# Performance work log

Measured on AMD Instinct MI355X. Metric: run time of the kernel, lower is better.

## Reference

```python
import jax, jax.numpy as jnp
import numpy as np

DIM = 4096
N_HEADS = 32
N_KV_HEADS = 8
HEAD_DIM = 128
ROPE_BASE = 10000.0
B, L = 4, 1024
NEG_INF = -1e9


def rope_traditional(x, base=ROPE_BASE, offset=0):
    # x: [B, H, L, Dh]; rotates interleaved pairs (x[...,2i], x[...,2i+1])
    Dh = x.shape[-1]
    Lx = x.shape[2]
    inv_freq = base ** (-jnp.arange(0, Dh, 2, dtype=jnp.float32) / Dh)  # [Dh/2]
    pos = jnp.arange(offset, offset + Lx, dtype=jnp.float32)
    ang = pos[:, None] * inv_freq  # [L, Dh/2]
    cos, sin = jnp.cos(ang), jnp.sin(ang)
    x1, x2 = x[..., ::2], x[..., 1::2]
    r1 = x1 * cos - x2 * sin
    r2 = x1 * sin + x2 * cos
    return jnp.stack([r1, r2], axis=-1).reshape(x.shape).astype(x.dtype)


def setup_inputs() -> dict:
    key = jax.random.key(0)
    ks = jax.random.split(key, 5)
    x = jax.random.normal(ks[0], (B, L, DIM), dtype=jnp.float32)
    # additive causal mask: 0 on/below diag, -inf-like above
    mask = jnp.where(jnp.tril(jnp.ones((L, L), dtype=bool)), 0.0, NEG_INF).astype(jnp.float32)
    wq = jax.random.normal(ks[1], (DIM, N_HEADS * HEAD_DIM), dtype=jnp.float32) * 0.02
    wk = jax.random.normal(ks[2], (DIM, N_KV_HEADS * HEAD_DIM), dtype=jnp.float32) * 0.02
    wv = jax.random.normal(ks[3], (DIM, N_KV_HEADS * HEAD_DIM), dtype=jnp.float32) * 0.02
    wo = jax.random.normal(ks[4], (N_HEADS * HEAD_DIM, DIM), dtype=jnp.float32) * 0.02
    return {"x": x, "mask": mask, "wq": wq, "wk": wk, "wv": wv, "wo": wo}


def reference(x, mask, wq, wk, wv, wo):
    Bx, Lx, D = x.shape
    scale = HEAD_DIM ** -0.5
    repeats = N_HEADS // N_KV_HEADS
    q = (x @ wq).reshape(Bx, Lx, N_HEADS, HEAD_DIM).transpose(0, 2, 1, 3)      # [B,H,L,Dh]
    k = (x @ wk).reshape(Bx, Lx, N_KV_HEADS, HEAD_DIM).transpose(0, 2, 1, 3)   # [B,Hkv,L,Dh]
    v = (x @ wv).reshape(Bx, Lx, N_KV_HEADS, HEAD_DIM).transpose(0, 2, 1, 3)
    # GQA expansion: head h attends to kv head h % n_kv_heads (matches
    # expand_dims+repeat(axis=1)+reshape in the original)
    k = jnp.tile(k, (1, repeats, 1, 1))  # [B,H,L,Dh]
    v = jnp.tile(v, (1, repeats, 1, 1))
    # cache=None path: rope with offset 0
    q = rope_traditional(q)
    k = rope_traditional(k)
    scores = jnp.einsum("bhqd,bhkd->bhqk", q * scale, k) + mask
    probs = jax.nn.softmax(scores.astype(jnp.float32), axis=-1).astype(scores.dtype)
    out = jnp.einsum("bhqk,bhkd->bhqd", probs, v)
    out = out.transpose(0, 2, 1, 3).reshape(Bx, Lx, D)
    return out @ wo
```

## Files before the change

### kernel.cpp

```cpp
#include <hip/hip_runtime.h>
#include <stdint.h>

typedef unsigned short u16;
typedef __bf16 bf16x8 __attribute__((ext_vector_type(8)));
typedef float f32x4 __attribute__((ext_vector_type(4)));

__device__ __forceinline__ u16 f2b(float x) {
  uint32_t b = __float_as_uint(x);
  b += 0x7fff + ((b >> 16) & 1);
  return (u16)(b >> 16);
}
__device__ __forceinline__ float b2f(u16 u) {
  return __uint_as_float(((uint32_t)u) << 16);
}

#define GLD16(src, dst)                                                                  \
  __builtin_amdgcn_global_load_lds((const __attribute__((address_space(1))) void*)(src),\
                                   (__attribute__((address_space(3))) void*)(dst), 16, 0, 0)

__device__ __forceinline__ f32x4 mfma16(bf16x8 a, bf16x8 b, f32x4 c) {
  return __builtin_amdgcn_mfma_f32_16x16x32_bf16(a, b, c, 0, 0, 0);
}

__global__ void k_rope_table(float2* __restrict__ tab) {
  int i = blockIdx.x * 256 + threadIdx.x;
  int l = i >> 6, d = i & 63;
  float inv = powf(10000.0f, -(float)(2 * d) / 128.0f);
  float ang = (float)l * inv;
  float s, c;
  sincosf(ang, &s, &c);
  tab[i] = make_float2(c, s);
}

__global__ void k_cast8(const float* __restrict__ src, u16* __restrict__ dst) {
  size_t i = (size_t)blockIdx.x * 256 + threadIdx.x;
  const float4* s4 = (const float4*)src;
  float4 a = s4[2 * i], b = s4[2 * i + 1];
  union { u16 u[8]; uint4 v; } o;
  o.u[0] = f2b(a.x); o.u[1] = f2b(a.y); o.u[2] = f2b(a.z); o.u[3] = f2b(a.w);
  o.u[4] = f2b(b.x); o.u[5] = f2b(b.y); o.u[6] = f2b(b.z); o.u[7] = f2b(b.w);
  ((uint4*)dst)[i] = o.v;
}

__global__ __launch_bounds__(256) void k_tcast(const float* __restrict__ src,
                                               u16* __restrict__ dst, int R, int C) {
  __shared__ u16 t[64][72];
  int tiles_c = C >> 6;
  int tr = blockIdx.x / tiles_c, tc = blockIdx.x % tiles_c;
  int tid = threadIdx.x;
  {
    int rr = tid >> 4, cv = tid & 15;
#pragma unroll
    for (int it = 0; it < 4; ++it) {
      int row = rr + it * 16;
      float4 v = *(const float4*)(src + (size_t)(tr * 64 + row) * C + tc * 64 + cv * 4);
      t[row][cv * 4 + 0] = f2b(v.x);
      t[row][cv * 4 + 1] = f2b(v.y);
      t[row][cv * 4 + 2] = f2b(v.z);
      t[row][cv * 4 + 3] = f2b(v.w);
    }
  }
  __syncthreads();
  {
    int cc = tid >> 3, g = tid & 7;
#pragma unroll
    for (int it = 0; it < 2; ++it) {
      int c = cc + it * 32;
      union { u16 u[8]; uint4 v; } o;
#pragma unroll
      for (int j = 0; j < 8; ++j) o.u[j] = t[g * 8 + j][c];
      *(uint4*)(dst + (size_t)(tc * 64 + c) * R + tr * 64 + g * 8) = o.v;
    }
  }
}

__global__ __launch_bounds__(256) void k_vtrans(const u16* __restrict__ qkv,
                                                u16* __restrict__ vrt) {
  __shared__ u16 t[64][72];
  int b = blockIdx.x >> 8;
  int tt = blockIdx.x & 255;
  int tr = tt >> 4, tc = tt & 15;
  int tid = threadIdx.x;
  {
    int rr = tid >> 3, g = tid & 7;
#pragma unroll
    for (int it = 0; it < 2; ++it) {
      int row = rr + it * 32;
      union { u16 u[8]; uint4 v; } o;
      o.v = *(const uint4*)(qkv + (size_t)(b * 1024 + tr * 64 + row) * 6144 + 5120 + tc * 64 + g * 8);
#pragma unroll
      for (int j = 0; j < 8; ++j) t[row][g * 8 + j] = o.u[j];
    }
  }
  __syncthreads();
  {
    int cc = tid >> 3, g = tid & 7;
#pragma unroll
    for (int it = 0; it < 2; ++it) {
      int c = cc + it * 32;
      union { u16 u[8]; uint4 v; } o;
#pragma unroll
      for (int j = 0; j < 8; ++j) o.u[j] = t[g * 8 + j][c];
      *(uint4*)(vrt + (size_t)(b * 1024 + tc * 64 + c) * 1024 + tr * 64 + g * 8) = o.v;
    }
  }
}

__global__ __launch_bounds__(320) void k_rope8(const u16* __restrict__ qkv,
                                               const float2* __restrict__ tab,
                                               u16* __restrict__ qr, u16* __restrict__ kr) {
  int row = blockIdx.x;
  int j = threadIdx.x * 8;
  int b = row >> 10, l = row & 1023;
  const float qs = 0.12751586584003446f;
  bool isq = (j < 2048);
  int jj = isq ? j : (j - 2048);
  int h = jj >> 6, dp = jj & 63;
  const u16* src = qkv + (size_t)row * 6144 + (isq ? 0 : 4096) + h * 128 + 2 * dp;
  uint4 v0 = *(const uint4*)(src);
  uint4 v1 = *(const uint4*)(src + 8);
  const float2* tb = tab + l * 64 + dp;
  float sc = isq ? qs : 1.0f;
  union { u16 u[16]; uint4 v[2]; } o;
  const uint32_t* w = (const uint32_t*)&v0;
#pragma unroll
  for (int i = 0; i < 8; ++i) {
    uint32_t pair = (i < 4) ? w[i] : ((const uint32_t*)&v1)[i - 4];
    float2 cs = tb[i];
    float x1 = b2f((u16)pair), x2 = b2f((u16)(pair >> 16));
    float r1 = (x1 * cs.x - x2 * cs.y) * sc;
    float r2 = (x1 * cs.y + x2 * cs.x) * sc;
    o.u[2 * i] = f2b(r1);
    o.u[2 * i + 1] = f2b(r2);
  }
  u16* dst = isq ? (qr + ((size_t)((b * 32 + h) * 1024 + l)) * 128 + 2 * dp)
                 : (kr + ((size_t)((b * 8 + h) * 1024 + l)) * 128 + 2 * dp);
  *(uint4*)(dst) = o.v[0];
  *(uint4*)(dst + 8) = o.v[1];
}

#define STAGE2(s0, s1, koff, ldsoff)          \
  GLD16((s0) + (koff), dst0 + (ldsoff));      \
  GLD16((s1) + (koff), dst1 + (ldsoff));

#define LOADB(base, kh)                                                   \
  bfr[0] = *(const bf16x8*)((base) + (kh) * 8192 + 0 * 512);              \
  bfr[1] = *(const bf16x8*)((base) + (kh) * 8192 + 1 * 512);              \
  bfr[2] = *(const bf16x8*)((base) + (kh) * 8192 + 2 * 512);              \
  bfr[3] = *(const bf16x8*)((base) + (kh) * 8192 + 3 * 512);

#define LOADA(base, kh, mh)                                               \
  afr[0] = *(const bf16x8*)((base) + (kh) * 8192 + (mh) * 2048 + 0 * 512);\
  afr[1] = *(const bf16x8*)((base) + (kh) * 8192 + (mh) * 2048 + 1 * 512);\
  afr[2] = *(const bf16x8*)((base) + (kh) * 8192 + (mh) * 2048 + 2 * 512);\
  afr[3] = *(const bf16x8*)((base) + (kh) * 8192 + (mh) * 2048 + 3 * 512);

#define PH(mh)                                                            \
  __builtin_amdgcn_s_barrier();                                           \
  asm volatile("s_waitcnt lgkmcnt(0)" ::: "memory");                      \
  __builtin_amdgcn_s_setprio(1);                                          \
  _Pragma("unroll") for (int mm = 0; mm < 4; ++mm)                        \
    _Pragma("unroll") for (int n_ = 0; n_ < 4; ++n_)                      \
      acc[(mh) * 4 + mm][n_] = mfma16(afr[mm], bfr[n_], acc[(mh) * 4 + mm][n_]); \
  __builtin_amdgcn_s_setprio(0);                                          \
  __builtin_amdgcn_s_barrier();

#define VMC(n) asm volatile("s_waitcnt vmcnt(" #n ")" ::: "memory");

template <typename OutT>
__global__ __launch_bounds__(512, 2) void k_gemm8(const u16* __restrict__ A,
                                                  const u16* __restrict__ Bt,
                                                  OutT* __restrict__ C,
                                                  int M, int N, int K) {
  extern __shared__ u16 lds[];
  const int tid = threadIdx.x;
  const int lane = tid & 63, wid = tid >> 6;
  const int l16 = lane & 15, lhi = lane >> 4;
  const int wm = wid >> 2, wn = wid & 3;

  const int nbn = N >> 8;
  int bid = blockIdx.x;
  const int cpx = gridDim.x >> 3;
  bid = (bid & 7) * cpx + (bid >> 3);
  const int bm = (bid / nbn) << 8;
  const int bn = (bid % nbn) << 8;

  const u16* Ag = A + (size_t)bm * K;
  const u16* Bg = Bt + (size_t)bn * K;

  const int swz = (lhi ^ ((l16 >> 1) & 3)) << 3;
  const u16* pA0 = lds + wm * 4096 + l16 * 32 + swz;
  const u16* pA1 = pA0 + 32768;
  const u16* pB0 = lds + 16384 + wn * 2048 + l16 * 32 + swz;
  const u16* pB1 = pB0 + 32768;

  const int r0 = tid >> 2, g0 = tid & 3;
  const int r1 = r0 + 128;
  const size_t so0 = (size_t)r0 * K + ((g0 ^ ((r0 >> 1) & 3)) << 3);
  const size_t so1 = (size_t)r1 * K + ((g0 ^ ((r1 >> 1) & 3)) << 3);
  const u16* sA0 = Ag + so0;
  const u16* sA1 = Ag + so1;
  const u16* sB0 = Bg + so0;
  const u16* sB1 = Bg + so1;
  u16* dst0 = lds + wid * 512;
  u16* dst1 = lds + 4096 + wid * 512;

  f32x4 acc[8][4] = {};
  bf16x8 bfr[4], afr[4];

  STAGE2(sA0, sA1, 0, 0);
  STAGE2(sA0, sA1, 32, 8192);
  STAGE2(sB0, sB1, 0, 16384);
  STAGE2(sB0, sB1, 32, 24576);
  STAGE2(sB0, sB1, 64, 49152);
  STAGE2(sA0, sA1, 64, 32768);
  STAGE2(sB0, sB1, 96, 57344);
  VMC(6)
  __builtin_amdgcn_s_barrier();

  const int nt = K >> 6;
  for (int t = 0; t < nt - 2; t += 2) {
    const int kA1 = (t + 1) * 64 + 32;
    const int k2 = (t + 2) * 64;
    const int k3 = (t + 3) * 64;
    LOADB(pB0, 0)
    LOADA(pA0, 0, 0)
    STAGE2(sA0, sA1, kA1, 40960);
    PH(0)
    LOADA(pA0, 0, 1)
    STAGE2(sB0, sB1, k2, 16384);
    PH(1)
    LOADB(pB0, 1)
    LOADA(pA0, 1, 0)
    STAGE2(sA0, sA1, k2, 0);
    PH(0)
    LOADA(pA0, 1, 1)
    STAGE2(sB0, sB1, k2 + 32, 24576);
    VMC(6)
    PH(1)
    LOADB(pB1, 0)
    LOADA(pA1, 0, 0)
    STAGE2(sA0, sA1, k2 + 32, 8192);
    PH(0)
    LOADA(pA1, 0, 1)
    STAGE2(sB0, sB1, k3, 49152);
    PH(1)
    LOADB(pB1, 1)
    LOADA(pA1, 1, 0)
    STAGE2(sA0, sA1, k3, 32768);
    PH(0)
    LOADA(pA1, 1, 1)
    STAGE2(sB0, sB1, k3 + 32, 57344);
    VMC(6)
    PH(1)
  }
  {
    const int kA1 = (nt - 1) * 64 + 32;
    LOADB(pB0, 0)
    LOADA(pA0, 0, 0)
    STAGE2(sA0, sA1, kA1, 40960);
    PH(0)
    LOADA(pA0, 0, 1)
    PH(1)
    LOADB(pB0, 1)
    LOADA(pA0, 1, 0)
    PH(0)
    LOADA(pA0, 1, 1)
    VMC(0)
    PH(1)
    LOADB(pB1, 0)
    LOADA(pA1, 0, 0)
    PH(0)
    LOADA(pA1, 0, 1)
    PH(1)
    LOADB(pB1, 1)
    LOADA(pA1, 1, 0)
    PH(0)
    LOADA(pA1, 1, 1)
    PH(1)
  }

#pragma unroll
  for (int m = 0; m < 8; ++m) {
    int row = bm + wm * 128 + m * 16 + lhi * 4;
#pragma unroll
    for (int n = 0; n < 4; ++n) {
      int col = bn + wn * 64 + n * 16 + l16;
#pragma unroll
      for (int r = 0; r < 4; ++r) {
        float v = acc[m][n][r];
        size_t idx = (size_t)(row + r) * N + col;
        if constexpr (sizeof(OutT) == 2) C[idx] = f2b(v);
        else C[idx] = v;
      }
    }
  }
}

__global__ __launch_bounds__(512) void k_attn(const u16* __restrict__ qr,
                                              const u16* __restrict__ kr,
                                              const u16* __restrict__ vrt,
                                              u16* __restrict__ ao) {
  __shared__ u16 Klds[8192];
  __shared__ u16 Vlds[8192];
  __shared__ u16 Plds[9216];
  int bid = blockIdx.x;
  int qb = bid & 7, h = (bid >> 3) & 31, b = bid >> 8;
  int kvh = h & 7;
  int lane = threadIdx.x & 63, w = threadIdx.x >> 6;
  int l16 = lane & 15, lhi = lane >> 4;
  int qmin = qb * 128 + w * 16;

  const u16* qbase = qr + ((size_t)((b * 32 + h) * 1024) + qmin + l16) * 128;
  bf16x8 aq[4];
#pragma unroll
  for (int kc = 0; kc < 4; ++kc) aq[kc] = *(const bf16x8*)(qbase + kc * 32 + lhi * 8);

  const u16* Kg = kr + (size_t)(b * 8 + kvh) * (1024 * 128);
  const u16* Vg = vrt + (size_t)(b * 8 + kvh) * (128 * 1024);

  float m_run[4] = {-1e30f, -1e30f, -1e30f, -1e30f};
  float l_part[4] = {0.f, 0.f, 0.f, 0.f};
  f32x4 o[8] = {};

  int nkb = 2 * qb + 2;
  for (int kb = 0; kb < nkb; ++kb) {
    int kv0 = kb * 64;
#pragma unroll
    for (int i = 0; i < 2; ++i) {
      int c = w * 128 + i * 64 + lane;
      int krow = c >> 4, g = c & 15;
      GLD16(Kg + (size_t)(kv0 + krow) * 128 + ((g ^ (krow & 7)) * 8),
            Klds + (w * 128 + i * 64) * 8);
    }
#pragma unroll
    for (int i = 0; i < 2; ++i) {
      int c = w * 128 + i * 64 + lane;
      int d = c >> 3, g = c & 7;
      GLD16(Vg + (size_t)d * 1024 + kv0 + ((g ^ (d & 7)) * 8),
            Vlds + (w * 128 + i * 64) * 8);
    }
    __syncthreads();

    f32x4 s[4] = {};
#pragma unroll
    for (int kc = 0; kc < 4; ++kc) {
#pragma unroll
      for (int n = 0; n < 4; ++n) {
        int kv = n * 16 + l16;
        int g = kc * 4 + lhi;
        bf16x8 bk = *(const bf16x8*)(Klds + kv * 128 + ((g ^ (kv & 7)) * 8));
        s[n] = mfma16(aq[kc], bk, s[n]);
      }
    }
    if (kv0 + 63 > qmin) {
#pragma unroll
      for (int n = 0; n < 4; ++n)
#pragma unroll
        for (int r = 0; r < 4; ++r) {
          int q = qmin + lhi * 4 + r;
          int kv = kv0 + n * 16 + l16;
          if (kv > q) s[n][r] = -1e30f;
        }
    }
    float mx[4];
    bool need = false;
#pragma unroll
    for (int r = 0; r < 4; ++r) {
      float m0 = fmaxf(fmaxf(s[0][r], s[1][r]), fmaxf(s[2][r], s[3][r]));
      m0 = fmaxf(m0, __shfl_xor(m0, 1));
      m0 = fmaxf(m0, __shfl_xor(m0, 2));
      m0 = fmaxf(m0, __shfl_xor(m0, 4));
      m0 = fmaxf(m0, __shfl_xor(m0, 8));
      mx[r] = m0;
      need = need || (m0 > m_run[r] + 11.0f);
    }
    if (__any(need)) {
#pragma unroll
      for (int r = 0; r < 4; ++r) {
        float mn = fmaxf(m_run[r], mx[r]);
        float sf = exp2f(m_run[r] - mn);
        m_run[r] = mn;
        l_part[r] *= sf;
#pragma unroll
        for (int nd = 0; nd < 8; ++nd) o[nd][r] *= sf;
      }
    }
    u16* pw = Plds + w * 1152;
#pragma unroll
    for (int r = 0; r < 4; ++r) {
      float lsum = 0.f;
#pragma unroll
      for (int n = 0; n < 4; ++n) {
        float p = exp2f(s[n][r] - m_run[r]);
        lsum += p;
        pw[(lhi * 4 + r) * 72 + n * 16 + l16] = f2b(p);
      }
      l_part[r] += lsum;
    }
#pragma unroll
    for (int kc = 0; kc < 2; ++kc) {
      bf16x8 ap = *(const bf16x8*)(pw + l16 * 72 + kc * 32 + lhi * 8);
#pragma unroll
      for (int nd = 0; nd < 8; ++nd) {
        int d = nd * 16 + l16;
        int g = kc * 4 + lhi;
        bf16x8 bv = *(const bf16x8*)(Vlds + d * 64 + ((g ^ (d & 7)) * 8));
        o[nd] = mfma16(ap, bv, o[nd]);
      }
    }
    __syncthreads();
  }
#pragma unroll
  for (int r = 0; r < 4; ++r) {
    float l = l_part[r];
    l += __shfl_xor(l, 1);
    l += __shfl_xor(l, 2);
    l += __shfl_xor(l, 4);
    l += __shfl_xor(l, 8);
    float inv = 1.0f / l;
    int q = qmin + lhi * 4 + r;
    u16* orow = ao + ((size_t)(b * 1024 + q)) * 4096 + h * 128;
#pragma unroll
    for (int nd = 0; nd < 8; ++nd) orow[nd * 16 + l16] = f2b(o[nd][r] * inv);
  }
}

extern "C" void kernel_launch(void* const* d_in, const int* in_sizes, int n_in,
                              void* d_out, int out_size, void* d_ws, size_t ws_size,
                              hipStream_t stream) {
  const float* x = (const float*)d_in[0];
  const float* wq = (const float*)d_in[2];
  const float* wk = (const float*)d_in[3];
  const float* wv = (const float*)d_in[4];
  const float* wo = (const float*)d_in[5];

  char* ws = (char*)d_ws;
  u16* xb = (u16*)(ws + 0);
  u16* wcat = (u16*)(ws + 33554432);
  u16* qr = (u16*)(ws + 0);
  u16* kr = (u16*)(ws + 33554432);
  u16* vrt = (u16*)(ws + 41943040);
  u16* ao = (u16*)(ws + 50331648);
  u16* wob = (u16*)(ws + 83886080);
  float2* tab = (float2*)(ws + 117440512);
  u16* qkv = (u16*)d_out;

  hipFuncSetAttribute((const void*)k_gemm8<u16>,
                      hipFuncAttributeMaxDynamicSharedMemorySize, 131072);
  hipFuncSetAttribute((const void*)k_gemm8<float>,
                      hipFuncAttributeMaxDynamicSharedMemorySize, 131072);

  k_rope_table<<<256, 256, 0, stream>>>(tab);
  k_cast8<<<8192, 256, 0, stream>>>(x, xb);
  k_tcast<<<4096, 256, 0, stream>>>(wq, wcat, 4096, 4096);
  k_tcast<<<1024, 256, 0, stream>>>(wk, wcat + (size_t)4096 * 4096, 4096, 1024);
  k_tcast<<<1024, 256, 0, stream>>>(wv, wcat + (size_t)5120 * 4096, 4096, 1024);
  k_tcast<<<4096, 256, 0, stream>>>(wo, wob, 4096, 4096);
  k_gemm8<u16><<<384, 512, 131072, stream>>>(xb, wcat, qkv, 4096, 6144, 4096);
  k_rope8<<<4096, 320, 0, stream>>>(qkv, tab, qr, kr);
  k_vtrans<<<1024, 256, 0, stream>>>(qkv, vrt);
  k_attn<<<1024, 512, 0, stream>>>(qr, kr, vrt, ao);
  k_gemm8<float><<<256, 512, 131072, stream>>>(ao, wob, (float*)d_out, 4096, 4096, 4096);
}
```

Before: 541.2 us.

## Double-buffer K tiles in LDS and read V directly from global memory

Loads of K tiles into LDS are now double-buffered: the next tile is prefetched while the current one is used, with a waitcnt and barrier at the end of each iteration. V is no longer staged in LDS and is read straight from global memory inside the PV MFMA loop, which frees the V buffer's LDS space. This hides K load latency and removes one barrier per iteration. In exchange, V reads become uncached-in-LDS global loads sitting on the MFMA critical path, repeated by every wave.

```diff
diff --git a/kernel.cpp b/kernel.cpp
--- a/kernel.cpp
+++ b/kernel.cpp
@@ -301,8 +301,7 @@
                                               const u16* __restrict__ kr,
                                               const u16* __restrict__ vrt,
                                               u16* __restrict__ ao) {
-  __shared__ u16 Klds[8192];
-  __shared__ u16 Vlds[8192];
+  __shared__ u16 Klds[16384];
   __shared__ u16 Plds[9216];
   int bid = blockIdx.x;
   int qb = bid & 7, h = (bid >> 3) & 31, b = bid >> 8;
@@ -319,28 +318,33 @@
   const u16* Kg = kr + (size_t)(b * 8 + kvh) * (1024 * 128);
   const u16* Vg = vrt + (size_t)(b * 8 + kvh) * (128 * 1024);
 
+  const int c0 = w * 128 + lane;
+  const int kr0 = c0 >> 4, g0s = c0 & 15;
+  const int c1 = c0 + 64;
+  const int kr1 = c1 >> 4, g1s = c1 & 15;
+  const size_t ko0 = (size_t)kr0 * 128 + ((g0s ^ (kr0 & 7)) * 8);
+  const size_t ko1 = (size_t)kr1 * 128 + ((g1s ^ (kr1 & 7)) * 8);
+  u16* kd0 = Klds + c0 * 8;
+  u16* kd1 = Klds + c1 * 8;
+
   float m_run[4] = {-1e30f, -1e30f, -1e30f, -1e30f};
   float l_part[4] = {0.f, 0.f, 0.f, 0.f};
   f32x4 o[8] = {};
 
   int nkb = 2 * qb + 2;
+  GLD16(Kg + ko0, kd0);
+  GLD16(Kg + ko1, kd1);
+  asm volatile("s_waitcnt vmcnt(0)" ::: "memory");
+  __builtin_amdgcn_s_barrier();
+
   for (int kb = 0; kb < nkb; ++kb) {
     int kv0 = kb * 64;
-#pragma unroll
-    for (int i = 0; i < 2; ++i) {
-      int c = w * 128 + i * 64 + lane;
-      int krow = c >> 4, g = c & 15;
-      GLD16(Kg + (size_t)(kv0 + krow) * 128 + ((g ^ (krow & 7)) * 8),
-            Klds + (w * 128 + i * 64) * 8);
-    }
-#pragma unroll
-    for (int i = 0; i < 2; ++i) {
-      int c = w * 128 + i * 64 + lane;
-      int d = c >> 3, g = c & 7;
-      GLD16(Vg + (size_t)d * 1024 + kv0 + ((g ^ (d & 7)) * 8),
-            Vlds + (w * 128 + i * 64) * 8);
-    }
-    __syncthreads();
+    const u16* Kb = Klds + (kb & 1) * 8192;
+    int nb = ((kb & 1) ^ 1) * 8192;
+    if (kb + 1 < nkb) {
+      GLD16(Kg + (size_t)(kv0 + 64) * 128 + ko0, kd0 + nb);
+      GLD16(Kg + (size_t)(kv0 + 64) * 128 + ko1, kd1 + nb);
+    }
 
     f32x4 s[4] = {};
 #pragma unroll
@@ -349,7 +353,7 @@
       for (int n = 0; n < 4; ++n) {
         int kv = n * 16 + l16;
         int g = kc * 4 + lhi;
-        bf16x8 bk = *(const bf16x8*)(Klds + kv * 128 + ((g ^ (kv & 7)) * 8));
+        bf16x8 bk = *(const bf16x8*)(Kb + kv * 128 + ((g ^ (kv & 7)) * 8));
         s[n] = mfma16(aq[kc], bk, s[n]);
       }
     }
@@ -404,12 +408,12 @@
 #pragma unroll
       for (int nd = 0; nd < 8; ++nd) {
         int d = nd * 16 + l16;
-        int g = kc * 4 + lhi;
-        bf16x8 bv = *(const bf16x8*)(Vlds + d * 64 + ((g ^ (d & 7)) * 8));
+        bf16x8 bv = *(const bf16x8*)(Vg + (size_t)d * 1024 + kv0 + (kc * 4 + lhi) * 8);
         o[nd] = mfma16(ap, bv, o[nd]);
       }
     }
-    __syncthreads();
+    asm volatile("s_waitcnt vmcnt(0)" ::: "memory");
+    __builtin_amdgcn_s_barrier();
   }
 #pragma unroll
   for (int r = 0; r < 4; ++r) {
```

New measurement: 702.0 us. 29.7% more time.
